# Kernel tuning notes

Hardware: AMD Instinct MI355X
Metric: run time of the kernel (lower is better)

The kernel has to match this reference:

```python
import jax, jax.numpy as jnp
import numpy as np

EMBED = 1024
HEADS = 16
HD = EMBED // HEADS
FF = 4096
EPS = 1e-5

def _layernorm(x, g, b):
    mu = jnp.mean(x, axis=-1, keepdims=True)
    var = jnp.mean(jnp.square(x - mu), axis=-1, keepdims=True)
    return (x - mu) * jax.lax.rsqrt(var + EPS) * g + b

def setup_inputs() -> dict:
    key = jax.random.key(0)
    ks = jax.random.split(key, 10)
    s = 0.02
    return {
        "x": jax.random.normal(ks[0], (4, 2048, EMBED), dtype=jnp.float32),
        "Wq": jax.random.normal(ks[1], (EMBED, EMBED), dtype=jnp.float32) * s,
        "Wk": jax.random.normal(ks[2], (EMBED, EMBED), dtype=jnp.float32) * s,
        "Wv": jax.random.normal(ks[3], (EMBED, EMBED), dtype=jnp.float32) * s,
        "Wo": jax.random.normal(ks[4], (EMBED, EMBED), dtype=jnp.float32) * s,
        "bo": jnp.zeros((EMBED,), dtype=jnp.float32),
        "W1": jax.random.normal(ks[5], (EMBED, FF), dtype=jnp.float32) * s,
        "b1": jnp.zeros((FF,), dtype=jnp.float32),
        "W2": jax.random.normal(ks[6], (FF, EMBED), dtype=jnp.float32) * s,
        "b2": jnp.zeros((EMBED,), dtype=jnp.float32),
        "g1": jnp.ones((EMBED,), dtype=jnp.float32),
        "be1": jnp.zeros((EMBED,), dtype=jnp.float32),
        "g2": jnp.ones((EMBED,), dtype=jnp.float32),
        "be2": jnp.zeros((EMBED,), dtype=jnp.float32),
    }

def reference(x, Wq, Wk, Wv, Wo, bo, W1, b1, W2, b2, g1, be1, g2, be2):
    B, T, _ = x.shape
    # --- pre-norm self-attention (dropout = identity in eval) ---
    h = _layernorm(x, g1, be1)
    q = (h @ Wq).reshape(B, T, HEADS, HD).transpose(0, 2, 1, 3)  # bhtd
    k = (h @ Wk).reshape(B, T, HEADS, HD).transpose(0, 2, 1, 3)
    v = (h @ Wv).reshape(B, T, HEADS, HD).transpose(0, 2, 1, 3)
    scores = jnp.einsum('bhid,bhjd->bhij', q, k) / jnp.sqrt(jnp.float32(HD))
    causal = jnp.tril(jnp.ones((T, T), dtype=bool))
    scores = jnp.where(causal[None, None], scores, -jnp.inf)
    attn = jax.nn.softmax(scores, axis=-1)
    out = jnp.einsum('bhij,bhjd->bhid', attn, v)
    out = out.transpose(0, 2, 1, 3).reshape(B, T, EMBED)
    out = out @ Wo + bo
    x = x + out
    # --- pre-norm GELU FFN ---
    h2 = _layernorm(x, g2, be2)
    ff = jax.nn.gelu(h2 @ W1 + b1, approximate=False) @ W2 + b2
    return x + ff
```

## Files before the change

### kernel.cpp

```cpp
#include <hip/hip_runtime.h>

typedef unsigned short u16;
typedef __attribute__((ext_vector_type(8))) short bf16x8;
typedef __attribute__((ext_vector_type(4))) float f32x4;

#define EMBED 1024
#define FFDIM 4096
#define SEQ   2048
#define NTOK  8192
#define ATT_C 0.18033688011112042f

__device__ __forceinline__ u16 f2bf(float f) {
  union { float f; unsigned int u; } c; c.f = f;
  unsigned int r = ((c.u >> 16) & 1u) + 0x7fffu;
  return (u16)((c.u + r) >> 16);
}

__device__ __forceinline__ unsigned cvtpk(float lo, float hi) {
  unsigned r;
  asm("v_cvt_pk_bf16_f32 %0, %1, %2" : "=v"(r) : "v"(lo), "v"(hi));
  return r;
}

__device__ __forceinline__ void gload16(const u16* g, u16* l) {
  __builtin_amdgcn_global_load_lds((const __attribute__((address_space(1))) void*)g,
                                   (__attribute__((address_space(3))) void*)l, 16, 0, 0);
}

__global__ __launch_bounds__(256) void wtrans(const float* __restrict__ W,
                                              u16* __restrict__ Wt, int K, int N) {
  __shared__ float tile[32][33];
  const int tx = threadIdx.x & 31, ty = threadIdx.x >> 5;
  const int n0 = blockIdx.x << 5, k0 = blockIdx.y << 5;
#pragma unroll
  for (int r = 0; r < 32; r += 8)
    tile[ty + r][tx] = W[(size_t)(k0 + ty + r) * N + n0 + tx];
  __syncthreads();
#pragma unroll
  for (int r = 0; r < 32; r += 8)
    Wt[(size_t)(n0 + ty + r) * K + k0 + tx] = f2bf(tile[tx][ty + r]);
}

__global__ __launch_bounds__(256) void vtrans(const u16* __restrict__ qkv,
                                              u16* __restrict__ Vt) {
  __shared__ u16 tile[32][33];
  const int tx = threadIdx.x & 31, ty = threadIdx.x >> 5;
  const int t0 = blockIdx.x << 5;
  const int rg0 = blockIdx.y << 5;
  const int bh = rg0 >> 6, d0 = rg0 & 63;
  const int b = bh >> 4, h = bh & 15;
#pragma unroll
  for (int r = 0; r < 32; r += 8)
    tile[ty + r][tx] = qkv[(size_t)(b * SEQ + t0 + ty + r) * 3072 + 2048 + h * 64 + d0 + tx];
  __syncthreads();
#pragma unroll
  for (int r = 0; r < 32; r += 8)
    Vt[(size_t)(rg0 + ty + r) * SEQ + t0 + tx] = tile[tx][ty + r];
}

__global__ __launch_bounds__(256) void ln_kernel(const float* __restrict__ xin,
                                                 const float* __restrict__ gamma,
                                                 const float* __restrict__ beta,
                                                 u16* __restrict__ out) {
  const int row = blockIdx.x, tid = threadIdx.x;
  const float4 v = reinterpret_cast<const float4*>(xin + (size_t)row * EMBED)[tid];
  float s  = v.x + v.y + v.z + v.w;
  float ss = v.x * v.x + v.y * v.y + v.z * v.z + v.w * v.w;
#pragma unroll
  for (int m = 1; m < 64; m <<= 1) { s += __shfl_xor(s, m); ss += __shfl_xor(ss, m); }
  __shared__ float red[8];
  if ((tid & 63) == 0) { red[tid >> 6] = s; red[4 + (tid >> 6)] = ss; }
  __syncthreads();
  s  = red[0] + red[1] + red[2] + red[3];
  ss = red[4] + red[5] + red[6] + red[7];
  const float mean = s * (1.0f / EMBED);
  const float var  = ss * (1.0f / EMBED) - mean * mean;
  const float rstd = rsqrtf(var + 1e-5f);
  const float4 g  = reinterpret_cast<const float4*>(gamma)[tid];
  const float4 bb = reinterpret_cast<const float4*>(beta)[tid];
  ushort4 o;
  o.x = f2bf((v.x - mean) * rstd * g.x + bb.x);
  o.y = f2bf((v.y - mean) * rstd * g.y + bb.y);
  o.z = f2bf((v.z - mean) * rstd * g.z + bb.z);
  o.w = f2bf((v.w - mean) * rstd * g.w + bb.w);
  reinterpret_cast<ushort4*>(out + (size_t)row * EMBED)[tid] = o;
}

template <int NREP, int EPI>
__global__ __launch_bounds__(512, 2) void gemm5(const u16* __restrict__ A,
                                                const u16* __restrict__ Bt,
                                                void* __restrict__ Cv,
                                                const float* __restrict__ bias,
                                                const float* __restrict__ res,
                                                int M, int N, int K) {
  constexpr int BN = NREP * 64;
  constexpr int GP = (NREP == 4) ? 4 : 3;
  __shared__ __align__(16) u16 As[2][256 * 64];
  __shared__ __align__(16) u16 Bs[2][BN * 64];

  const int tid = threadIdx.x;
  const int lane = tid & 63, wid = tid >> 6;
  const int l4 = lane >> 4, l15 = lane & 15;
  const int wq = wid >> 2, wn = wid & 3;

  const int gx = gridDim.x;
  const int nwg = gx * (int)gridDim.y;
  const int flat = (int)blockIdx.y * gx + (int)blockIdx.x;
  const int cpx = nwg >> 3;
  const int swz = (flat & 7) * cpx + (flat >> 3);
  const int brow = (swz / gx) << 8;
  const int bcol = (swz % gx) * BN;

  const f32x4 z4 = {0.f, 0.f, 0.f, 0.f};
  f32x4 acc[4][4][NREP / 2];
#pragma unroll
  for (int q = 0; q < 4; ++q)
#pragma unroll
    for (int m = 0; m < 4; ++m)
#pragma unroll
      for (int n = 0; n < NREP / 2; ++n) acc[q][m][n] = z4;

  const int srow = tid >> 3;
  const int scolb = ((tid & 7) << 4) ^ ((srow & 7) << 4);
  const u16* gAs = A  + (size_t)(brow + srow) * K + (scolb >> 1);
  const u16* gBs = Bt + (size_t)(bcol + srow) * K + (scolb >> 1);
  const int lA = wid * 512;

  const int nk = K >> 6;

#define STAGE_A(c_, t_, h_)                                                     \
  do {                                                                          \
    gload16(gAs + (size_t)((h_) * 128) * K + (size_t)(t_) * 64,                 \
            &As[c_][(h_) * 8192 + lA]);                                         \
    gload16(gAs + (size_t)((h_) * 128 + 64) * K + (size_t)(t_) * 64,            \
            &As[c_][(h_) * 8192 + 4096 + lA]);                                  \
  } while (0)
#define STAGE_B(c_, t_, h_)                                                     \
  do {                                                                          \
    if constexpr (NREP == 4) {                                                  \
      gload16(gBs + (size_t)((h_) * 128) * K + (size_t)(t_) * 64,               \
              &Bs[c_][(h_) * 8192 + lA]);                                       \
      gload16(gBs + (size_t)((h_) * 128 + 64) * K + (size_t)(t_) * 64,          \
              &Bs[c_][(h_) * 8192 + 4096 + lA]);                                \
    } else {                                                                    \
      gload16(gBs + (size_t)((h_) * 64) * K + (size_t)(t_) * 64,                \
              &Bs[c_][(h_) * 4096 + lA]);                                       \
    }                                                                           \
  } while (0)

  const int kk0  = l4 << 3;
  const int aswz = (l15 & 7) << 3;

#define RD_A(MH)                                                                \
  _Pragma("unroll")                                                             \
  for (int m_ = 0; m_ < 4; ++m_)                                                \
    _Pragma("unroll")                                                           \
    for (int ks_ = 0; ks_ < 2; ++ks_)                                           \
      af[m_][ks_] = *(const bf16x8*)&As[c][((MH) * 128 + wq * 64 + m_ * 16 + l15) * 64 + ((kk0 + ks_ * 32) ^ aswz)];
#define RD_B(NH)                                                                \
  _Pragma("unroll")                                                             \
  for (int n_ = 0; n_ < NREP / 2; ++n_)                                         \
    _Pragma("unroll")                                                           \
    for (int ks_ = 0; ks_ < 2; ++ks_)                                           \
      bf[n_][ks_] = *(const bf16x8*)&Bs[c][((NH) * (BN / 2) + wn * (BN / 8) + n_ * 16 + l15) * 64 + ((kk0 + ks_ * 32) ^ aswz)];
#define GATE_LG                                                                 \
  __builtin_amdgcn_s_barrier();                                                 \
  asm volatile("s_waitcnt lgkmcnt(0)" ::: "memory");                            \
  __builtin_amdgcn_sched_barrier(0)
#define MFMA_Q(Q_)                                                              \
  __builtin_amdgcn_s_setprio(1);                                                \
  _Pragma("unroll")                                                             \
  for (int m_ = 0; m_ < 4; ++m_)                                                \
    _Pragma("unroll")                                                           \
    for (int n_ = 0; n_ < NREP / 2; ++n_)                                       \
      _Pragma("unroll")                                                         \
      for (int ks_ = 0; ks_ < 2; ++ks_)                                         \
        acc[Q_][m_][n_] = __builtin_amdgcn_mfma_f32_16x16x32_bf16(              \
            af[m_][ks_], bf[n_][ks_], acc[Q_][m_][n_], 0, 0, 0);                \
  __builtin_amdgcn_s_setprio(0);

  bf16x8 af[4][2], bf[NREP / 2][2];

  STAGE_A(0, 0, 0);
  STAGE_B(0, 0, 0);
  STAGE_B(0, 0, 1);
  STAGE_A(0, 0, 1);
  if (nk > 1) { STAGE_A(1, 1, 0); STAGE_B(1, 1, 1); }
  asm volatile("s_waitcnt vmcnt(%0)" :: "i"(GP) : "memory");
  __builtin_amdgcn_s_barrier();

  for (int t = 0; t < nk; ++t) {
    const int c = t & 1, cn = c ^ 1;
    RD_A(0); RD_B(0);
    if (t + 1 < nk) STAGE_B(cn, t + 1, 0);
    if constexpr (NREP == 4) asm volatile("s_waitcnt lgkmcnt(8)" ::: "memory");
    GATE_LG;
    MFMA_Q(0);
    __builtin_amdgcn_s_barrier();
    RD_B(1);
    if (t + 1 < nk) STAGE_A(cn, t + 1, 1);
    GATE_LG;
    MFMA_Q(1);
    __builtin_amdgcn_s_barrier();
    RD_A(1);
    if (t + 2 < nk) STAGE_A(c, t + 2, 0);
    GATE_LG;
    MFMA_Q(2);
    __builtin_amdgcn_s_barrier();
    RD_B(0);
    if (t + 2 < nk) STAGE_B(c, t + 2, 1);
    GATE_LG;
    MFMA_Q(3);
    if (t + 2 < nk) {
      asm volatile("s_waitcnt vmcnt(%0)" :: "i"(GP) : "memory");
    } else {
      asm volatile("s_waitcnt vmcnt(0)" ::: "memory");
    }
    __builtin_amdgcn_s_barrier();
  }

#undef STAGE_A
#undef STAGE_B
#undef RD_A
#undef RD_B
#undef GATE_LG
#undef MFMA_Q

#pragma unroll
  for (int q = 0; q < 4; ++q) {
    const int mh = q >> 1, nh = (q >> 1) ^ (q & 1);
    const int rowb = brow + mh * 128 + wq * 64 + (l4 << 2);
    const int colb = bcol + nh * (BN / 2) + wn * (BN / 8) + l15;
#pragma unroll
    for (int n = 0; n < NREP / 2; ++n) {
      const int col = colb + n * 16;
      float bv = 0.f;
      if (EPI != 0) bv = bias[col];
#pragma unroll
      for (int m = 0; m < 4; ++m) {
#pragma unroll
        for (int j = 0; j < 4; ++j) {
          const int row = rowb + m * 16 + j;
          const float v = acc[q][m][n][j];
          if (EPI == 0) {
            ((u16*)Cv)[(size_t)row * N + col] = f2bf(v);
          } else if (EPI == 1) {
            ((float*)Cv)[(size_t)row * N + col] = v + bv + res[(size_t)row * N + col];
          } else {
            const float t2 = v + bv;
            const float gl = 0.5f * t2 * (1.0f + erff(t2 * 0.70710678118654752f));
            ((u16*)Cv)[(size_t)row * N + col] = f2bf(gl);
          }
        }
      }
    }
  }
}

__global__ __launch_bounds__(512) void attn_fwd(const u16* __restrict__ qkv,
                                                const u16* __restrict__ Vt,
                                                u16* __restrict__ attn) {
  __shared__ __align__(16) u16 Ks[64 * 72];
  __shared__ __align__(16) u16 Vs[64 * 72];
  __shared__ __align__(16) u16 Ps[8 * 16 * 72];
  const int tid = threadIdx.x, lane = tid & 63, wid = tid >> 6;
  const int l4 = lane >> 4, l15 = lane & 15;
  const int bh = blockIdx.y, b = bh >> 4, h = bh & 15;
  const size_t bt0 = (size_t)b * SEQ;
  u16* Pw = &Ps[wid * 16 * 72];

  const int sr = tid >> 3;
  const int sc0 = (tid & 7) << 3;
  const u16* kbase = qkv + bt0 * 3072 + 1024 + h * 64;
  const u16* vbase = Vt + (size_t)bh * 64 * SEQ;
  const f32x4 z4 = {0.f, 0.f, 0.f, 0.f};

#pragma unroll
  for (int ph = 0; ph < 2; ++ph) {
    const int Qb = ((ph == 0) ? (int)blockIdx.x : 15 - (int)blockIdx.x) << 7;
    const int qw = Qb + wid * 16;
    const int qlane = qw + l15;

    const u16* qp = qkv + (bt0 + qlane) * 3072 + h * 64 + (l4 << 3);
    const bf16x8 aq0 = *(const bf16x8*)qp;
    const bf16x8 aq1 = *(const bf16x8*)(qp + 32);

    f32x4 o[4];
#pragma unroll
    for (int dt = 0; dt < 4; ++dt) o[dt] = z4;
    float mrun = -1e30f, lrun = 0.f;

    bf16x8 kp = *(const bf16x8*)(kbase + (size_t)sr * 3072 + sc0);
    bf16x8 vp = *(const bf16x8*)(vbase + (size_t)sr * SEQ + sc0);

    const int jend = Qb + 128;
    for (int j0 = 0; j0 < jend; j0 += 64) {
      __syncthreads();
      *(bf16x8*)&Ks[sr * 72 + sc0] = kp;
      *(bf16x8*)&Vs[sr * 72 + sc0] = vp;
      __syncthreads();

      if (j0 + 64 < jend) {
        kp = *(const bf16x8*)(kbase + (size_t)(j0 + 64 + sr) * 3072 + sc0);
        vp = *(const bf16x8*)(vbase + (size_t)sr * SEQ + j0 + 64 + sc0);
      }

      if (j0 > qw + 15) continue;
      const int nt = min(4, ((qw + 15 - j0) >> 4) + 1);

      f32x4 s[4];
#pragma unroll
      for (int t = 0; t < 4; ++t) {
        if (t < nt) {
          const bf16x8 ak0 = *(const bf16x8*)&Ks[(t * 16 + l15) * 72 + (l4 << 3)];
          const bf16x8 ak1 = *(const bf16x8*)&Ks[(t * 16 + l15) * 72 + 32 + (l4 << 3)];
          f32x4 a = z4;
          a = __builtin_amdgcn_mfma_f32_16x16x32_bf16(ak0, aq0, a, 0, 0, 0);
          a = __builtin_amdgcn_mfma_f32_16x16x32_bf16(ak1, aq1, a, 0, 0, 0);
          s[t] = a;
        }
      }

      float mt = -1e30f;
#pragma unroll
      for (int t = 0; t < 4; ++t) {
        if (t < nt) {
          if (j0 + t * 16 + 15 > qw) {
            const int kvb = j0 + t * 16 + (l4 << 2);
#pragma unroll
            for (int j = 0; j < 4; ++j)
              if (kvb + j > qlane) s[t][j] = -1e30f;
          }
          mt = fmaxf(mt, fmaxf(fmaxf(s[t][0], s[t][1]), fmaxf(s[t][2], s[t][3])));
        }
      }
      mt = fmaxf(mt, __shfl_xor(mt, 16));
      mt = fmaxf(mt, __shfl_xor(mt, 32));

      const bool skip = __all(mt <= mrun + 44.0f);
      float scq = 1.0f;
      if (!skip) {
        const float mn = fmaxf(mrun, mt);
        scq = exp2f((mrun - mn) * ATT_C);
        mrun = mn;
      }
      const float mc = mrun * ATT_C;

      float ls = 0.f;
      uint2 pw[4];
#pragma unroll
      for (int t = 0; t < 4; ++t) {
        if (t < nt) {
          const float p0 = exp2f(__builtin_fmaf(s[t][0], ATT_C, -mc));
          const float p1 = exp2f(__builtin_fmaf(s[t][1], ATT_C, -mc));
          const float p2 = exp2f(__builtin_fmaf(s[t][2], ATT_C, -mc));
          const float p3 = exp2f(__builtin_fmaf(s[t][3], ATT_C, -mc));
          ls += (p0 + p1) + (p2 + p3);
          pw[t].x = cvtpk(p0, p1);
          pw[t].y = cvtpk(p2, p3);
        } else {
          pw[t].x = 0u; pw[t].y = 0u;
        }
      }
#pragma unroll
      for (int t = 0; t < 4; ++t)
        *(uint2*)&Pw[l15 * 72 + t * 16 + (l4 << 2)] = pw[t];

      ls += __shfl_xor(ls, 16);
      ls += __shfl_xor(ls, 32);

      if (!skip) {
        lrun = lrun * scq + ls;
#pragma unroll
        for (int dt = 0; dt < 4; ++dt)
#pragma unroll
          for (int j = 0; j < 4; ++j) o[dt][j] *= scq;
      } else {
        lrun += ls;
      }

      const int nc = (nt + 1) >> 1;
#pragma unroll
      for (int c = 0; c < 2; ++c) {
        if (c < nc) {
          const bf16x8 ap = *(const bf16x8*)&Pw[l15 * 72 + c * 32 + (l4 << 3)];
#pragma unroll
          for (int dt = 0; dt < 4; ++dt) {
            const bf16x8 bv = *(const bf16x8*)&Vs[(dt * 16 + l15) * 72 + c * 32 + (l4 << 3)];
            o[dt] = __builtin_amdgcn_mfma_f32_16x16x32_bf16(bv, ap, o[dt], 0, 0, 0);
          }
        }
      }
    }

    const float rl = 1.0f / lrun;
#pragma unroll
    for (int dt = 0; dt < 4; ++dt) {
      uint2 w;
      w.x = cvtpk(o[dt][0] * rl, o[dt][1] * rl);
      w.y = cvtpk(o[dt][2] * rl, o[dt][3] * rl);
      *(uint2*)&Pw[l15 * 72 + dt * 16 + (l4 << 2)] = w;
    }
#pragma unroll
    for (int rep = 0; rep < 2; ++rep) {
      const int unit = rep * 64 + lane;
      const int r = unit >> 3, c = unit & 7;
      const bf16x8 v = *(const bf16x8*)&Pw[r * 72 + c * 8];
      *(bf16x8*)&attn[(bt0 + qw + r) * EMBED + h * 64 + c * 8] = v;
    }
  }
}

extern "C" void kernel_launch(void* const* d_in, const int* in_sizes, int n_in,
                              void* d_out, int out_size, void* d_ws, size_t ws_size,
                              hipStream_t stream) {
  const float* x   = (const float*)d_in[0];
  const float* Wq  = (const float*)d_in[1];
  const float* Wk  = (const float*)d_in[2];
  const float* Wv  = (const float*)d_in[3];
  const float* Wo  = (const float*)d_in[4];
  const float* bo  = (const float*)d_in[5];
  const float* W1  = (const float*)d_in[6];
  const float* b1  = (const float*)d_in[7];
  const float* W2  = (const float*)d_in[8];
  const float* b2  = (const float*)d_in[9];
  const float* g1  = (const float*)d_in[10];
  const float* be1 = (const float*)d_in[11];
  const float* g2  = (const float*)d_in[12];
  const float* be2 = (const float*)d_in[13];

  char* ws = (char*)d_ws;
  u16* wqkv_t = (u16*)(ws + 0);
  u16* wo_t   = (u16*)(ws + 6291456);
  u16* w1_t   = (u16*)(ws + 8388608);
  u16* w2_t   = (u16*)(ws + 16777216);
  u16* hbuf   = (u16*)(ws + 25165824);
  u16* qkv    = (u16*)(ws + 41943040);
  u16* ff1    = (u16*)(ws + 41943040);
  u16* vt     = (u16*)(ws + 92274688);
  u16* attnb  = (u16*)(ws + 109051904);
  float* x2   = (float*)(ws + 125829120);
  float* outp = (float*)d_out;

  dim3 blk(256);
  wtrans<<<dim3(32, 32),  blk, 0, stream>>>(Wq, wqkv_t,               1024, 1024);
  wtrans<<<dim3(32, 32),  blk, 0, stream>>>(Wk, wqkv_t + 1024 * 1024, 1024, 1024);
  wtrans<<<dim3(32, 32),  blk, 0, stream>>>(Wv, wqkv_t + 2048 * 1024, 1024, 1024);
  wtrans<<<dim3(32, 32),  blk, 0, stream>>>(Wo, wo_t,                 1024, 1024);
  wtrans<<<dim3(128, 32), blk, 0, stream>>>(W1, w1_t,                 1024, 4096);
  wtrans<<<dim3(32, 128), blk, 0, stream>>>(W2, w2_t,                 4096, 1024);

  ln_kernel<<<dim3(8192), blk, 0, stream>>>(x, g1, be1, hbuf);
  gemm5<2, 0><<<dim3(24, 32), dim3(512), 0, stream>>>(hbuf, wqkv_t, qkv, nullptr, nullptr,
                                                      8192, 3072, 1024);
  vtrans<<<dim3(64, 128), blk, 0, stream>>>(qkv, vt);
  attn_fwd<<<dim3(8, 64), dim3(512), 0, stream>>>(qkv, vt, attnb);
  gemm5<2, 1><<<dim3(8, 32), dim3(512), 0, stream>>>(attnb, wo_t, x2, bo, x,
                                                     8192, 1024, 1024);
  ln_kernel<<<dim3(8192), blk, 0, stream>>>(x2, g2, be2, hbuf);
  gemm5<4, 2><<<dim3(16, 32), dim3(512), 0, stream>>>(hbuf, w1_t, ff1, b1, nullptr,
                                                      8192, 4096, 1024);
  gemm5<2, 1><<<dim3(8, 32), dim3(512), 0, stream>>>(ff1, w2_t, outp, b2, x2,
                                                     8192, 1024, 4096);
}
```

Measured before the change: 425.7 us.

## Restructure GEMM main loop into two phases with double B fragments

The four-phase GEMM k-loop, which prefetched two k-tiles ahead, becomes a two-phase loop that prefetches only one tile ahead. Both B half-fragments are held in separate register sets so each phase issues two MFMA quadrants. This halves the barriers and LDS read gates per k-step. The cost is more live registers and a shorter prefetch distance, which may expose more global load latency.

Result: faster. 414.2 us (-2.7%).

```diff
diff --git a/kernel.cpp b/kernel.cpp
--- a/kernel.cpp
+++ b/kernel.cpp
@@ -87,14 +87,14 @@
 }
 
 template <int NREP, int EPI>
-__global__ __launch_bounds__(512, 2) void gemm5(const u16* __restrict__ A,
+__global__ __launch_bounds__(512, 2) void gemm7(const u16* __restrict__ A,
                                                 const u16* __restrict__ Bt,
                                                 void* __restrict__ Cv,
                                                 const float* __restrict__ bias,
                                                 const float* __restrict__ res,
                                                 int M, int N, int K) {
   constexpr int BN = NREP * 64;
-  constexpr int GP = (NREP == 4) ? 4 : 3;
+  constexpr int VH = (NREP == 4) ? 6 : 4;
   __shared__ __align__(16) u16 As[2][256 * 64];
   __shared__ __align__(16) u16 Bs[2][BN * 64];
 
@@ -157,18 +157,18 @@
     _Pragma("unroll")                                                           \
     for (int ks_ = 0; ks_ < 2; ++ks_)                                           \
       af[m_][ks_] = *(const bf16x8*)&As[c][((MH) * 128 + wq * 64 + m_ * 16 + l15) * 64 + ((kk0 + ks_ * 32) ^ aswz)];
-#define RD_B(NH)                                                                \
+#define RD_B(DST, NH)                                                           \
   _Pragma("unroll")                                                             \
   for (int n_ = 0; n_ < NREP / 2; ++n_)                                         \
     _Pragma("unroll")                                                           \
     for (int ks_ = 0; ks_ < 2; ++ks_)                                           \
-      bf[n_][ks_] = *(const bf16x8*)&Bs[c][((NH) * (BN / 2) + wn * (BN / 8) + n_ * 16 + l15) * 64 + ((kk0 + ks_ * 32) ^ aswz)];
+      DST[n_][ks_] = *(const bf16x8*)&Bs[c][((NH) * (BN / 2) + wn * (BN / 8) + n_ * 16 + l15) * 64 + ((kk0 + ks_ * 32) ^ aswz)];
 #define GATE_LG                                                                 \
   __builtin_amdgcn_s_barrier();                                                 \
   asm volatile("s_waitcnt lgkmcnt(0)" ::: "memory");                            \
   __builtin_amdgcn_sched_barrier(0)
-#define MFMA_Q(Q_)                                                              \
-  __builtin_amdgcn_s_setprio(1);                                                \
+#define VM(N_) asm volatile("s_waitcnt vmcnt(%0)" :: "i"(N_) : "memory")
+#define MFMA_Q(Q_, BF_)                                                         \
   _Pragma("unroll")                                                             \
   for (int m_ = 0; m_ < 4; ++m_)                                                \
     _Pragma("unroll")                                                           \
@@ -176,46 +176,36 @@
       _Pragma("unroll")                                                         \
       for (int ks_ = 0; ks_ < 2; ++ks_)                                         \
         acc[Q_][m_][n_] = __builtin_amdgcn_mfma_f32_16x16x32_bf16(              \
-            af[m_][ks_], bf[n_][ks_], acc[Q_][m_][n_], 0, 0, 0);                \
-  __builtin_amdgcn_s_setprio(0);
-
-  bf16x8 af[4][2], bf[NREP / 2][2];
+            af[m_][ks_], BF_[n_][ks_], acc[Q_][m_][n_], 0, 0, 0);
+
+  bf16x8 af[4][2], bf0[NREP / 2][2], bf1[NREP / 2][2];
 
   STAGE_A(0, 0, 0);
   STAGE_B(0, 0, 0);
   STAGE_B(0, 0, 1);
   STAGE_A(0, 0, 1);
-  if (nk > 1) { STAGE_A(1, 1, 0); STAGE_B(1, 1, 1); }
-  asm volatile("s_waitcnt vmcnt(%0)" :: "i"(GP) : "memory");
+  VM(2);
   __builtin_amdgcn_s_barrier();
 
   for (int t = 0; t < nk; ++t) {
     const int c = t & 1, cn = c ^ 1;
-    RD_A(0); RD_B(0);
-    if (t + 1 < nk) STAGE_B(cn, t + 1, 0);
-    if constexpr (NREP == 4) asm volatile("s_waitcnt lgkmcnt(8)" ::: "memory");
+    RD_A(0); RD_B(bf0, 0); RD_B(bf1, 1);
+    if (t + 1 < nk) { STAGE_B(cn, t + 1, 0); STAGE_B(cn, t + 1, 1); STAGE_A(cn, t + 1, 0); }
     GATE_LG;
-    MFMA_Q(0);
+    __builtin_amdgcn_s_setprio(1);
+    MFMA_Q(0, bf0);
+    MFMA_Q(1, bf1);
+    __builtin_amdgcn_s_setprio(0);
     __builtin_amdgcn_s_barrier();
-    RD_B(1);
+    if (t + 1 < nk) { VM(VH); } else { VM(0); }
+    RD_A(1);
     if (t + 1 < nk) STAGE_A(cn, t + 1, 1);
     GATE_LG;
-    MFMA_Q(1);
-    __builtin_amdgcn_s_barrier();
-    RD_A(1);
-    if (t + 2 < nk) STAGE_A(c, t + 2, 0);
-    GATE_LG;
-    MFMA_Q(2);
-    __builtin_amdgcn_s_barrier();
-    RD_B(0);
-    if (t + 2 < nk) STAGE_B(c, t + 2, 1);
-    GATE_LG;
-    MFMA_Q(3);
-    if (t + 2 < nk) {
-      asm volatile("s_waitcnt vmcnt(%0)" :: "i"(GP) : "memory");
-    } else {
-      asm volatile("s_waitcnt vmcnt(0)" ::: "memory");
-    }
+    __builtin_amdgcn_s_setprio(1);
+    MFMA_Q(2, bf1);
+    MFMA_Q(3, bf0);
+    __builtin_amdgcn_s_setprio(0);
+    VM(2);
     __builtin_amdgcn_s_barrier();
   }
 
@@ -224,6 +214,7 @@
 #undef RD_A
 #undef RD_B
 #undef GATE_LG
+#undef VM
 #undef MFMA_Q
 
 #pragma unroll
@@ -451,15 +442,15 @@
   wtrans<<<dim3(32, 128), blk, 0, stream>>>(W2, w2_t,                 4096, 1024);
 
   ln_kernel<<<dim3(8192), blk, 0, stream>>>(x, g1, be1, hbuf);
-  gemm5<2, 0><<<dim3(24, 32), dim3(512), 0, stream>>>(hbuf, wqkv_t, qkv, nullptr, nullptr,
+  gemm7<2, 0><<<dim3(24, 32), dim3(512), 0, stream>>>(hbuf, wqkv_t, qkv, nullptr, nullptr,
                                                       8192, 3072, 1024);
   vtrans<<<dim3(64, 128), blk, 0, stream>>>(qkv, vt);
   attn_fwd<<<dim3(8, 64), dim3(512), 0, stream>>>(qkv, vt, attnb);
-  gemm5<2, 1><<<dim3(8, 32), dim3(512), 0, stream>>>(attnb, wo_t, x2, bo, x,
+  gemm7<2, 1><<<dim3(8, 32), dim3(512), 0, stream>>>(attnb, wo_t, x2, bo, x,
                                                      8192, 1024, 1024);
   ln_kernel<<<dim3(8192), blk, 0, stream>>>(x2, g2, be2, hbuf);
-  gemm5<4, 2><<<dim3(16, 32), dim3(512), 0, stream>>>(hbuf, w1_t, ff1, b1, nullptr,
+  gemm7<4, 2><<<dim3(16, 32), dim3(512), 0, stream>>>(hbuf, w1_t, ff1, b1, nullptr,
                                                       8192, 4096, 1024);
-  gemm5<2, 1><<<dim3(8, 32), dim3(512), 0, stream>>>(ff1, w2_t, outp, b2, x2,
+  gemm7<2, 1><<<dim3(8, 32), dim3(512), 0, stream>>>(ff1, w2_t, outp, b2, x2,
                                                      8192, 1024, 4096);
 }
```
